# Kernel tuning notes

Measured on AMD Instinct MI355X. Metric: run time of the kernel, lower is better.

The kernel has to match this reference:

```python
import jax, jax.numpy as jnp
import numpy as np
from math import sqrt

B, S, H, NH = 4, 1024, 1024, 16
HS = H // NH
ALPHA = 2.0


def apply_rope(x, dis):
    # x: [B,S,NH,HS], dis: [B,S,1,HS] = [sin || cos]
    dis_sin, dis_cos = jnp.split(dis, 2, axis=-1)
    x0, x1 = x[..., 0::2], x[..., 1::2]
    return jnp.concatenate([x0 * dis_cos - x1 * dis_sin,
                            x1 * dis_cos + x0 * dis_sin], axis=-1)


def setup_inputs() -> dict:
    key = jax.random.key(0)
    ks = jax.random.split(key, 12)
    tgt = jax.random.normal(ks[0], (B, S, H), dtype=jnp.float32)
    # causal mask so every softmax row has at least one valid key
    tgt_mask = jnp.tril(jnp.ones((S, S), dtype=bool))[None, None]  # [1,1,S,S]
    tgt_mask = jnp.broadcast_to(tgt_mask, (B, 1, S, S))
    glycan_mass = jax.random.uniform(ks[1], (B, S, 1, HS), dtype=jnp.float32)
    glycan_query_mass = jax.random.uniform(ks[2], (B, S, 1, HS), dtype=jnp.float32)
    s = 1.0 / np.sqrt(H)
    Wq = jax.random.normal(ks[3], (H, H), dtype=jnp.float32) * s
    Wk = jax.random.normal(ks[4], (H, H), dtype=jnp.float32) * s
    Wv = jax.random.normal(ks[5], (H, H), dtype=jnp.float32) * (0.5 * s)  # beta gain
    Wo = jax.random.normal(ks[6], (H, H), dtype=jnp.float32) * (0.5 * s)
    bq = jnp.zeros((H,), jnp.float32)
    bk = jnp.zeros((H,), jnp.float32)
    bv = jnp.zeros((H,), jnp.float32)
    bo = jnp.zeros((H,), jnp.float32)
    ln_w = jnp.ones((H,), jnp.float32)
    ln_b = jnp.zeros((H,), jnp.float32)
    return {"tgt": tgt, "tgt_mask": tgt_mask, "glycan_mass": glycan_mass,
            "glycan_query_mass": glycan_query_mass,
            "Wq": Wq, "bq": bq, "Wk": Wk, "bk": bk, "Wv": Wv, "bv": bv,
            "Wo": Wo, "bo": bo, "ln_w": ln_w, "ln_b": ln_b}


def reference(tgt, tgt_mask, glycan_mass, glycan_query_mass,
              Wq, bq, Wk, bk, Wv, bv, Wo, bo, ln_w, ln_b):
    b = tgt.shape[0]
    q = (tgt @ Wq + bq).reshape(b, -1, NH, HS)
    k = (tgt @ Wk + bk).reshape(b, -1, NH, HS)
    v = (tgt @ Wv + bv).reshape(b, -1, NH, HS)
    q = apply_rope(q, glycan_query_mass)
    k = apply_rope(k, glycan_mass)
    # attn: [b, head, q_pos, k_pos]
    attn = jnp.einsum('bnij,bmij->binm', q, k) / sqrt(HS)
    attn = jnp.where(tgt_mask, attn, -jnp.inf)
    attn = jax.nn.softmax(attn, axis=-1)
    postx = jnp.einsum('binm,bmij->bnij', attn, v).reshape(b, -1, H)
    postx = postx @ Wo + bo
    # DeepNorm (dropout = identity at inference)
    x = tgt * ALPHA + postx
    mu = jnp.mean(x, axis=-1, keepdims=True)
    var = jnp.var(x, axis=-1, keepdims=True)
    return (x - mu) / jnp.sqrt(var + 1e-5) * ln_w + ln_b
```

## Files before the change

kernel.cpp:

```cpp
#include <hip/hip_runtime.h>

#define NB 4
#define NS 1024
#define NHID 1024
#define NHEAD 16
#define HDIM 64

typedef unsigned short u16;
typedef __bf16 bf16x8 __attribute__((ext_vector_type(8)));
typedef float f32x4 __attribute__((ext_vector_type(4)));
typedef u16 us8 __attribute__((ext_vector_type(8)));
typedef u16 us4 __attribute__((ext_vector_type(4)));

__device__ __forceinline__ u16 f2b(float f) {
  union { float f; unsigned u; } v; v.f = f;
  unsigned r = v.u + 0x7fffu + ((v.u >> 16) & 1u);
  return (u16)(r >> 16);
}
__device__ __forceinline__ float b2f(u16 b) {
  union { unsigned u; float f; } v; v.u = ((unsigned)b) << 16;
  return v.f;
}
__device__ __forceinline__ bf16x8 as_bf(us8 v) {
  bf16x8 r; __builtin_memcpy(&r, &v, sizeof(r)); return r;
}

__global__ void k_wt(const float* __restrict__ Wq, const float* __restrict__ Wk,
                     const float* __restrict__ Wv, const float* __restrict__ Wo,
                     u16* __restrict__ out) {
  const float* W = (blockIdx.z == 0) ? Wq : (blockIdx.z == 1) ? Wk
                   : (blockIdx.z == 2) ? Wv : Wo;
  u16* o = out + (size_t)blockIdx.z * NHID * NHID;
  __shared__ u16 tl[64][65];
  const int n0 = blockIdx.x * 64, k0 = blockIdx.y * 64;
  const int tr = threadIdx.x >> 4, tc = (threadIdx.x & 15) * 4;
#pragma unroll
  for (int rr = tr; rr < 64; rr += 16) {
    float4 v = *(const float4*)(W + (size_t)(k0 + rr) * NHID + n0 + tc);
    tl[rr][tc + 0] = f2b(v.x);
    tl[rr][tc + 1] = f2b(v.y);
    tl[rr][tc + 2] = f2b(v.z);
    tl[rr][tc + 3] = f2b(v.w);
  }
  __syncthreads();
#pragma unroll
  for (int rr = tr; rr < 64; rr += 16) {
    us4 v;
    v[0] = tl[tc + 0][rr];
    v[1] = tl[tc + 1][rr];
    v[2] = tl[tc + 2][rr];
    v[3] = tl[tc + 3][rr];
    *(us4*)(o + (size_t)(n0 + rr) * NHID + k0 + tc) = v;
  }
}

__global__ __launch_bounds__(256, 2) void k_gemm_qkv(
    const float* __restrict__ tgt, const u16* __restrict__ Wt,
    const float* __restrict__ bq, const float* __restrict__ bk,
    const float* __restrict__ bv, u16* __restrict__ Qb, u16* __restrict__ Kb,
    u16* __restrict__ VTb) {
  const int z = blockIdx.z;
  const u16* Wz = Wt + (size_t)z * NHID * NHID;
  const float* bias = (z == 0) ? bq : (z == 1) ? bk : bv;
  const bool vt = (z == 2);
  const int m0 = (vt ? blockIdx.x : blockIdx.y) * 128;
  const int n0 = (vt ? blockIdx.y : blockIdx.x) * 128;

  __shared__ u16 As[128 * 64];
  __shared__ u16 Bs[128 * 64];

  const int t = threadIdx.x;
  const int w = t >> 6, lane = t & 63, lq = lane & 15, lk = lane >> 4;
  const int wm = (w >> 1) * 64, wn = (w & 1) * 64;

  f32x4 acc[4][4];
#pragma unroll
  for (int i = 0; i < 4; i++)
#pragma unroll
    for (int j = 0; j < 4; j++) acc[i][j] = (f32x4){0.f, 0.f, 0.f, 0.f};

  for (int k0 = 0; k0 < NHID; k0 += 64) {
    __syncthreads();
#pragma unroll
    for (int i = 0; i < 4; i++) {
      int idx = t + i * 256;
      int r = idx >> 3, ch = idx & 7;
      us8 va, vb;
      if (!vt) {
        const float* ap = tgt + (size_t)(m0 + r) * NHID + k0 + ch * 8;
        float4 a0 = *(const float4*)ap;
        float4 a1 = *(const float4*)(ap + 4);
        va[0] = f2b(a0.x); va[1] = f2b(a0.y); va[2] = f2b(a0.z); va[3] = f2b(a0.w);
        va[4] = f2b(a1.x); va[5] = f2b(a1.y); va[6] = f2b(a1.z); va[7] = f2b(a1.w);
        vb = *(const us8*)(Wz + (size_t)(n0 + r) * NHID + k0 + ch * 8);
      } else {
        va = *(const us8*)(Wz + (size_t)(m0 + r) * NHID + k0 + ch * 8);
        const float* bp = tgt + (size_t)(n0 + r) * NHID + k0 + ch * 8;
        float4 b0 = *(const float4*)bp;
        float4 b1 = *(const float4*)(bp + 4);
        vb[0] = f2b(b0.x); vb[1] = f2b(b0.y); vb[2] = f2b(b0.z); vb[3] = f2b(b0.w);
        vb[4] = f2b(b1.x); vb[5] = f2b(b1.y); vb[6] = f2b(b1.z); vb[7] = f2b(b1.w);
      }
      *(us8*)(As + r * 64 + ((ch ^ (r & 7)) << 3)) = va;
      *(us8*)(Bs + r * 64 + ((ch ^ (r & 7)) << 3)) = vb;
    }
    __syncthreads();
#pragma unroll
    for (int kk = 0; kk < 2; kk++) {
      bf16x8 af[4], bfv[4];
#pragma unroll
      for (int m = 0; m < 4; m++) {
        int r = wm + m * 16 + lq;
        int ch = kk * 4 + lk;
        af[m] = as_bf(*(const us8*)(As + r * 64 + ((ch ^ (r & 7)) << 3)));
      }
#pragma unroll
      for (int n = 0; n < 4; n++) {
        int r = wn + n * 16 + lq;
        int ch = kk * 4 + lk;
        bfv[n] = as_bf(*(const us8*)(Bs + r * 64 + ((ch ^ (r & 7)) << 3)));
      }
#pragma unroll
      for (int m = 0; m < 4; m++)
#pragma unroll
        for (int n = 0; n < 4; n++)
          acc[m][n] = __builtin_amdgcn_mfma_f32_16x16x32_bf16(af[m], bfv[n],
                                                              acc[m][n], 0, 0, 0);
    }
  }
  if (!vt) {
#pragma unroll
    for (int m = 0; m < 4; m++)
#pragma unroll
      for (int n = 0; n < 4; n++) {
        int gn = n0 + wn + n * 16 + lq;
        int h = gn >> 6, d = gn & 63;
        float bval = bias[gn];
#pragma unroll
        for (int r = 0; r < 4; r++) {
          int gm = m0 + wm + m * 16 + 4 * lk + r;
          int b = gm >> 10, s = gm & 1023;
          float v = acc[m][n][r] + bval;
          ((z == 0) ? Qb : Kb)[(((size_t)(b * NHEAD + h) * NS + s) << 6) + d] =
              f2b(v);
        }
      }
  } else {
#pragma unroll
    for (int m = 0; m < 4; m++)
#pragma unroll
      for (int n = 0; n < 4; n++) {
        int gn = n0 + wn + n * 16 + lq;
        int b = gn >> 10, s = gn & 1023;
#pragma unroll
        for (int r = 0; r < 4; r++) {
          int gm = m0 + wm + m * 16 + 4 * lk + r;
          int h = gm >> 6, d = gm & 63;
          float v = acc[m][n][r] + bias[gm];
          VTb[(((size_t)(b * NHEAD + h)) << 16) + ((size_t)d << 10) + s] = f2b(v);
        }
      }
  }
}

__global__ void k_rope(u16* __restrict__ Qb, u16* __restrict__ Kb,
                       const float* __restrict__ qmass,
                       const float* __restrict__ kmass) {
  int id = blockIdx.x * 256 + threadIdx.x;
  int which = id >> 16;
  int r = id & 65535;
  int s = r & 1023;
  int b = r >> 14;
  u16* ptr = (which ? Kb : Qb) + ((size_t)r << 6);
  const float* dis = (which ? kmass : qmass) + ((size_t)(b * NS + s) << 6);
  float x[64];
#pragma unroll
  for (int c8 = 0; c8 < 8; c8++) {
    us8 v = *(const us8*)(ptr + c8 * 8);
#pragma unroll
    for (int j = 0; j < 8; j++) x[c8 * 8 + j] = b2f(v[j]);
  }
  us8 outv[8];
#pragma unroll
  for (int c = 0; c < 32; c++) {
    float sn = dis[c], cs = dis[32 + c];
    float x0 = x[2 * c], x1 = x[2 * c + 1];
    outv[c >> 3][c & 7] = f2b(x0 * cs - x1 * sn);
    outv[(c >> 3) + 4][c & 7] = f2b(x1 * cs + x0 * sn);
  }
#pragma unroll
  for (int c8 = 0; c8 < 8; c8++) *(us8*)(ptr + c8 * 8) = outv[c8];
}

__global__ __launch_bounds__(256, 2) void k_attn(const u16* __restrict__ Qb,
                                                 const u16* __restrict__ Kb,
                                                 const u16* __restrict__ VTb,
                                                 u16* __restrict__ Ob) {
  const int id = blockIdx.x;
  const int wrk = (id & 7) * 128 + (id >> 3);
  const int bh = wrk >> 4;
  const int qt = 15 - (wrk & 15);
  const int b = bh >> 4, h = bh & 15;
  const size_t hoff = (size_t)bh << 16;
  const u16* Qh = Qb + hoff;
  const u16* Kh = Kb + hoff;
  const u16* VTh = VTb + hoff;

  __shared__ u16 Ps[4][1024];

  const int t = threadIdx.x, w = t >> 6, lane = t & 63;
  const int lq = lane & 15, lk = lane >> 4;

  bf16x8 qf[2];
  {
    const u16* qr = Qh + (size_t)(qt * 64 + w * 16 + lq) * 64;
    qf[0] = as_bf(*(const us8*)(qr + lk * 8));
    qf[1] = as_bf(*(const us8*)(qr + 32 + lk * 8));
  }

  f32x4 oacc[4];
#pragma unroll
  for (int i = 0; i < 4; i++) oacc[i] = (f32x4){0.f, 0.f, 0.f, 0.f};
  float mrun[4] = {-1e30f, -1e30f, -1e30f, -1e30f};
  float lrun[4] = {0.f, 0.f, 0.f, 0.f};

  for (int kt = 0; kt <= qt; ++kt) {
    const u16* kb = Kh + ((size_t)kt << 12);
    us8 kfr[4][2];
#pragma unroll
    for (int fc = 0; fc < 4; fc++)
#pragma unroll
      for (int kk = 0; kk < 2; kk++)
        kfr[fc][kk] =
            *(const us8*)(kb + (fc * 16 + lq) * 64 + (kk * 4 + lk) * 8);
    us8 vfr[4][2];
#pragma unroll
    for (int fc = 0; fc < 4; fc++)
#pragma unroll
      for (int kk = 0; kk < 2; kk++)
        vfr[fc][kk] = *(const us8*)(VTh + ((size_t)(fc * 16 + lq) << 10) +
                                    kt * 64 + (kk * 4 + lk) * 8);

    f32x4 sfr[4];
#pragma unroll
    for (int fc = 0; fc < 4; fc++) {
      f32x4 a = (f32x4){0.f, 0.f, 0.f, 0.f};
#pragma unroll
      for (int kk = 0; kk < 2; kk++)
        a = __builtin_amdgcn_mfma_f32_16x16x32_bf16(qf[kk], as_bf(kfr[fc][kk]),
                                                    a, 0, 0, 0);
      sfr[fc] = a;
    }
    const float sc = 0.125f;
    if (kt == qt) {
#pragma unroll
      for (int fc = 0; fc < 4; fc++)
#pragma unroll
        for (int r = 0; r < 4; r++) {
          int qrow = w * 16 + 4 * lk + r;
          int kcol = fc * 16 + lq;
          sfr[fc][r] = (kcol <= qrow) ? sfr[fc][r] * sc : -1e30f;
        }
    } else {
#pragma unroll
      for (int fc = 0; fc < 4; fc++)
#pragma unroll
        for (int r = 0; r < 4; r++) sfr[fc][r] *= sc;
    }
    float pv[4][4];
#pragma unroll
    for (int r = 0; r < 4; r++) {
      float mx = fmaxf(fmaxf(sfr[0][r], sfr[1][r]), fmaxf(sfr[2][r], sfr[3][r]));
#pragma unroll
      for (int d = 1; d < 16; d <<= 1) mx = fmaxf(mx, __shfl_xor(mx, d));
      float mn = fmaxf(mrun[r], mx);
      float corr = __expf(mrun[r] - mn);
      float rs = 0.f;
#pragma unroll
      for (int fc = 0; fc < 4; fc++) {
        float p = __expf(sfr[fc][r] - mn);
        pv[fc][r] = p;
        rs += p;
      }
#pragma unroll
      for (int d = 1; d < 16; d <<= 1) rs += __shfl_xor(rs, d);
      mrun[r] = mn;
      lrun[r] = lrun[r] * corr + rs;
#pragma unroll
      for (int fc = 0; fc < 4; fc++) oacc[fc][r] *= corr;
    }
    u16* Pw = Ps[w];
#pragma unroll
    for (int fc = 0; fc < 4; fc++)
#pragma unroll
      for (int r = 0; r < 4; r++) {
        int i = 4 * lk + r, c = fc * 16 + lq;
        Pw[i * 64 + (((c >> 3) ^ (i & 7)) << 3) + (c & 7)] = f2b(pv[fc][r]);
      }
    bf16x8 pf[2];
#pragma unroll
    for (int kk = 0; kk < 2; kk++) {
      int ch = kk * 4 + lk;
      pf[kk] = as_bf(*(const us8*)(Pw + lq * 64 + ((ch ^ (lq & 7)) << 3)));
    }
#pragma unroll
    for (int fc = 0; fc < 4; fc++)
#pragma unroll
      for (int kk = 0; kk < 2; kk++)
        oacc[fc] = __builtin_amdgcn_mfma_f32_16x16x32_bf16(
            pf[kk], as_bf(vfr[fc][kk]), oacc[fc], 0, 0, 0);
  }
#pragma unroll
  for (int fc = 0; fc < 4; fc++)
#pragma unroll
    for (int r = 0; r < 4; r++) {
      int qrow = qt * 64 + w * 16 + 4 * lk + r;
      float o = oacc[fc][r] / lrun[r];
      Ob[((size_t)(b * NS + qrow) << 10) + h * 64 + fc * 16 + lq] = f2b(o);
    }
}

__global__ __launch_bounds__(256, 2) void k_gemm_o(
    const u16* __restrict__ Ab, const u16* __restrict__ Wz,
    const float* __restrict__ bo, const float* __restrict__ tgt,
    u16* __restrict__ xb) {
  __shared__ u16 As[128 * 64];
  __shared__ u16 Bs[128 * 64];

  const int t = threadIdx.x;
  const int m0 = blockIdx.y * 128, n0 = blockIdx.x * 128;
  const int w = t >> 6, lane = t & 63, lq = lane & 15, lk = lane >> 4;
  const int wm = (w >> 1) * 64, wn = (w & 1) * 64;

  f32x4 acc[4][4];
#pragma unroll
  for (int i = 0; i < 4; i++)
#pragma unroll
    for (int j = 0; j < 4; j++) acc[i][j] = (f32x4){0.f, 0.f, 0.f, 0.f};

  for (int k0 = 0; k0 < NHID; k0 += 64) {
    __syncthreads();
#pragma unroll
    for (int i = 0; i < 4; i++) {
      int idx = t + i * 256;
      int r = idx >> 3, ch = idx & 7;
      us8 va = *(const us8*)(Ab + (size_t)(m0 + r) * NHID + k0 + ch * 8);
      *(us8*)(As + r * 64 + ((ch ^ (r & 7)) << 3)) = va;
      us8 vb = *(const us8*)(Wz + (size_t)(n0 + r) * NHID + k0 + ch * 8);
      *(us8*)(Bs + r * 64 + ((ch ^ (r & 7)) << 3)) = vb;
    }
    __syncthreads();
#pragma unroll
    for (int kk = 0; kk < 2; kk++) {
      bf16x8 af[4], bfv[4];
#pragma unroll
      for (int m = 0; m < 4; m++) {
        int r = wm + m * 16 + lq;
        int ch = kk * 4 + lk;
        af[m] = as_bf(*(const us8*)(As + r * 64 + ((ch ^ (r & 7)) << 3)));
      }
#pragma unroll
      for (int n = 0; n < 4; n++) {
        int r = wn + n * 16 + lq;
        int ch = kk * 4 + lk;
        bfv[n] = as_bf(*(const us8*)(Bs + r * 64 + ((ch ^ (r & 7)) << 3)));
      }
#pragma unroll
      for (int m = 0; m < 4; m++)
#pragma unroll
        for (int n = 0; n < 4; n++)
          acc[m][n] = __builtin_amdgcn_mfma_f32_16x16x32_bf16(af[m], bfv[n],
                                                              acc[m][n], 0, 0, 0);
    }
  }
#pragma unroll
  for (int m = 0; m < 4; m++)
#pragma unroll
    for (int n = 0; n < 4; n++) {
      int gn = n0 + wn + n * 16 + lq;
      float bval = bo[gn];
#pragma unroll
      for (int r = 0; r < 4; r++) {
        int gm = m0 + wm + m * 16 + 4 * lk + r;
        float v = acc[m][n][r] + bval + 2.0f * tgt[((size_t)gm << 10) + gn];
        xb[((size_t)gm << 10) + gn] = f2b(v);
      }
    }
}

__global__ void k_ln(const u16* __restrict__ xb, const float* __restrict__ lw,
                     const float* __restrict__ lb, float* __restrict__ out) {
  const int row = blockIdx.x, t = threadIdx.x;
  const u16* xr = xb + ((size_t)row << 10);
  us4 v = *(const us4*)(xr + t * 4);
  float f[4];
  float s = 0.f, sq = 0.f;
#pragma unroll
  for (int j = 0; j < 4; j++) {
    f[j] = b2f(v[j]);
    s += f[j];
    sq += f[j] * f[j];
  }
#pragma unroll
  for (int d = 1; d < 64; d <<= 1) {
    s += __shfl_xor(s, d);
    sq += __shfl_xor(sq, d);
  }
  __shared__ float ss[4], sk[4];
  int w = t >> 6, lane = t & 63;
  if (lane == 0) {
    ss[w] = s;
    sk[w] = sq;
  }
  __syncthreads();
  s = ss[0] + ss[1] + ss[2] + ss[3];
  sq = sk[0] + sk[1] + sk[2] + sk[3];
  float mean = s * (1.0f / 1024.0f);
  float var = sq * (1.0f / 1024.0f) - mean * mean;
  float rstd = rsqrtf(var + 1e-5f);
  float4 o;
#pragma unroll
  for (int j = 0; j < 4; j++) {
    int c = t * 4 + j;
    ((float*)&o)[j] = (f[j] - mean) * rstd * lw[c] + lb[c];
  }
  *(float4*)(out + ((size_t)row << 10) + t * 4) = o;
}

extern "C" void kernel_launch(void* const* d_in, const int* in_sizes, int n_in,
                              void* d_out, int out_size, void* d_ws,
                              size_t ws_size, hipStream_t stream) {
  const float* tgt = (const float*)d_in[0];
  const float* kmass = (const float*)d_in[2];
  const float* qmass = (const float*)d_in[3];
  const float* Wq = (const float*)d_in[4];
  const float* bq = (const float*)d_in[5];
  const float* Wk = (const float*)d_in[6];
  const float* bk = (const float*)d_in[7];
  const float* Wv = (const float*)d_in[8];
  const float* bv = (const float*)d_in[9];
  const float* Wo = (const float*)d_in[10];
  const float* bo = (const float*)d_in[11];
  const float* lw = (const float*)d_in[12];
  const float* lb = (const float*)d_in[13];
  float* out = (float*)d_out;

  char* ws = (char*)d_ws;
  u16* Wt = (u16*)ws;
  u16* Qb = (u16*)(ws + (8u << 20));
  u16* Kb = (u16*)(ws + (16u << 20));
  u16* VTb = (u16*)(ws + (24u << 20));
  u16* Ob = (u16*)(ws + (32u << 20));
  u16* xb = (u16*)(ws + (8u << 20));

  k_wt<<<dim3(16, 16, 4), 256, 0, stream>>>(Wq, Wk, Wv, Wo, Wt);
  k_gemm_qkv<<<dim3(8, 32, 3), 256, 0, stream>>>(tgt, Wt, bq, bk, bv, Qb, Kb,
                                                 VTb);
  k_rope<<<512, 256, 0, stream>>>(Qb, Kb, qmass, kmass);
  k_attn<<<1024, 256, 0, stream>>>(Qb, Kb, VTb, Ob);
  k_gemm_o<<<dim3(8, 32), 256, 0, stream>>>(Ob, Wt + 3u * NHID * NHID, bo, tgt,
                                            xb);
  k_ln<<<4096, 256, 0, stream>>>(xb, lw, lb, out);
}
```

Measured before the change: 304.5 us.

## Transpose attention MFMA operands so each lane owns one query row

The attention kernel swaps the MFMA operand order so the score and output tiles are transposed, with each lane holding a single query row. Row max and sum reductions then need two cross-lane shuffles instead of four per row, the per-row softmax state shrinks to scalars, and P is written to shared memory as packed 8-byte stores. Work is also split per wave on 16-row query tiles rather than per block on 64-row tiles, so each wave stops at its own causal bound and finishes with vectorized output stores. In exchange, waves in one block run loops of different lengths, and K/V fragments are still reloaded from global memory by every wave.

```diff
diff --git a/kernel.cpp b/kernel.cpp
--- a/kernel.cpp
+++ b/kernel.cpp
@@ -198,22 +198,24 @@
                                                  u16* __restrict__ Ob) {
   const int id = blockIdx.x;
   const int wrk = (id & 7) * 128 + (id >> 3);
-  const int bh = wrk >> 4;
-  const int qt = 15 - (wrk & 15);
+  const int w = threadIdx.x >> 6, lane = threadIdx.x & 63;
+  const int item = wrk * 4 + w;
+  const int bh = item >> 6;
+  const int qt16 = 63 - (item & 63);
   const int b = bh >> 4, h = bh & 15;
   const size_t hoff = (size_t)bh << 16;
   const u16* Qh = Qb + hoff;
   const u16* Kh = Kb + hoff;
   const u16* VTh = VTb + hoff;
-
-  __shared__ u16 Ps[4][1024];
-
-  const int t = threadIdx.x, w = t >> 6, lane = t & 63;
   const int lq = lane & 15, lk = lane >> 4;
+
+  __shared__ u16 Ps[4 * 16 * 64];
+  char* Prow = (char*)(Ps + (w * 16 + lq) * 64);
+  const unsigned swz = (unsigned)((lq & 7) << 4);
 
   bf16x8 qf[2];
   {
-    const u16* qr = Qh + (size_t)(qt * 64 + w * 16 + lq) * 64;
+    const u16* qr = Qh + (size_t)(qt16 * 16 + lq) * 64;
     qf[0] = as_bf(*(const us8*)(qr + lk * 8));
     qf[1] = as_bf(*(const us8*)(qr + 32 + lk * 8));
   }
@@ -221,10 +223,13 @@
   f32x4 oacc[4];
 #pragma unroll
   for (int i = 0; i < 4; i++) oacc[i] = (f32x4){0.f, 0.f, 0.f, 0.f};
-  float mrun[4] = {-1e30f, -1e30f, -1e30f, -1e30f};
-  float lrun[4] = {0.f, 0.f, 0.f, 0.f};
-
-  for (int kt = 0; kt <= qt; ++kt) {
+  float mrun = -1e30f, lrun = 0.f;
+
+  const int ktmax = qt16 >> 2;
+  const int qg = qt16 * 16 + lq;
+  const float sc = 0.125f;
+
+  for (int kt = 0; kt <= ktmax; ++kt) {
     const u16* kb = Kh + ((size_t)kt << 12);
     us8 kfr[4][2];
 #pragma unroll
@@ -232,14 +237,14 @@
 #pragma unroll
       for (int kk = 0; kk < 2; kk++)
         kfr[fc][kk] =
-            *(const us8*)(kb + (fc * 16 + lq) * 64 + (kk * 4 + lk) * 8);
+            *(const us8*)(kb + (fc * 16 + lq) * 64 + kk * 32 + lk * 8);
     us8 vfr[4][2];
 #pragma unroll
     for (int fc = 0; fc < 4; fc++)
 #pragma unroll
       for (int kk = 0; kk < 2; kk++)
         vfr[fc][kk] = *(const us8*)(VTh + ((size_t)(fc * 16 + lq) << 10) +
-                                    kt * 64 + (kk * 4 + lk) * 8);
+                                    kt * 64 + kk * 32 + lk * 8);
 
     f32x4 sfr[4];
 #pragma unroll
@@ -247,19 +252,17 @@
       f32x4 a = (f32x4){0.f, 0.f, 0.f, 0.f};
 #pragma unroll
       for (int kk = 0; kk < 2; kk++)
-        a = __builtin_amdgcn_mfma_f32_16x16x32_bf16(qf[kk], as_bf(kfr[fc][kk]),
+        a = __builtin_amdgcn_mfma_f32_16x16x32_bf16(as_bf(kfr[fc][kk]), qf[kk],
                                                     a, 0, 0, 0);
       sfr[fc] = a;
     }
-    const float sc = 0.125f;
-    if (kt == qt) {
+    if (kt == ktmax) {
 #pragma unroll
       for (int fc = 0; fc < 4; fc++)
 #pragma unroll
         for (int r = 0; r < 4; r++) {
-          int qrow = w * 16 + 4 * lk + r;
-          int kcol = fc * 16 + lq;
-          sfr[fc][r] = (kcol <= qrow) ? sfr[fc][r] * sc : -1e30f;
+          int kg = kt * 64 + fc * 16 + 4 * lk + r;
+          sfr[fc][r] = (kg <= qg) ? sfr[fc][r] * sc : -1e30f;
         }
     } else {
 #pragma unroll
@@ -267,57 +270,61 @@
 #pragma unroll
         for (int r = 0; r < 4; r++) sfr[fc][r] *= sc;
     }
-    float pv[4][4];
-#pragma unroll
-    for (int r = 0; r < 4; r++) {
-      float mx = fmaxf(fmaxf(sfr[0][r], sfr[1][r]), fmaxf(sfr[2][r], sfr[3][r]));
-#pragma unroll
-      for (int d = 1; d < 16; d <<= 1) mx = fmaxf(mx, __shfl_xor(mx, d));
-      float mn = fmaxf(mrun[r], mx);
-      float corr = __expf(mrun[r] - mn);
-      float rs = 0.f;
-#pragma unroll
-      for (int fc = 0; fc < 4; fc++) {
+    float tm = sfr[0][0];
+#pragma unroll
+    for (int fc = 0; fc < 4; fc++)
+#pragma unroll
+      for (int r = 0; r < 4; r++) tm = fmaxf(tm, sfr[fc][r]);
+    tm = fmaxf(tm, __shfl_xor(tm, 16));
+    tm = fmaxf(tm, __shfl_xor(tm, 32));
+    const float mn = fmaxf(mrun, tm);
+    const float corr = __expf(mrun - mn);
+    mrun = mn;
+    float pvv[4][4];
+    float rs = 0.f;
+#pragma unroll
+    for (int fc = 0; fc < 4; fc++)
+#pragma unroll
+      for (int r = 0; r < 4; r++) {
         float p = __expf(sfr[fc][r] - mn);
-        pv[fc][r] = p;
+        pvv[fc][r] = p;
         rs += p;
       }
-#pragma unroll
-      for (int d = 1; d < 16; d <<= 1) rs += __shfl_xor(rs, d);
-      mrun[r] = mn;
-      lrun[r] = lrun[r] * corr + rs;
-#pragma unroll
-      for (int fc = 0; fc < 4; fc++) oacc[fc][r] *= corr;
-    }
-    u16* Pw = Ps[w];
-#pragma unroll
-    for (int fc = 0; fc < 4; fc++)
-#pragma unroll
-      for (int r = 0; r < 4; r++) {
-        int i = 4 * lk + r, c = fc * 16 + lq;
-        Pw[i * 64 + (((c >> 3) ^ (i & 7)) << 3) + (c & 7)] = f2b(pv[fc][r]);
-      }
+    rs += __shfl_xor(rs, 16);
+    rs += __shfl_xor(rs, 32);
+    lrun = lrun * corr + rs;
+#pragma unroll
+    for (int fc = 0; fc < 4; fc++) oacc[fc] *= corr;
+
+#pragma unroll
+    for (int fc = 0; fc < 4; fc++) {
+      uint2 pk;
+      pk.x = (unsigned)f2b(pvv[fc][0]) | ((unsigned)f2b(pvv[fc][1]) << 16);
+      pk.y = (unsigned)f2b(pvv[fc][2]) | ((unsigned)f2b(pvv[fc][3]) << 16);
+      *(uint2*)(Prow + (((unsigned)(fc * 32 + lk * 8)) ^ swz)) = pk;
+    }
     bf16x8 pf[2];
 #pragma unroll
-    for (int kk = 0; kk < 2; kk++) {
-      int ch = kk * 4 + lk;
-      pf[kk] = as_bf(*(const us8*)(Pw + lq * 64 + ((ch ^ (lq & 7)) << 3)));
-    }
+    for (int kk = 0; kk < 2; kk++)
+      pf[kk] = as_bf(
+          *(const us8*)(Prow + (((unsigned)(kk * 64 + lk * 16)) ^ swz)));
+
 #pragma unroll
     for (int fc = 0; fc < 4; fc++)
 #pragma unroll
       for (int kk = 0; kk < 2; kk++)
         oacc[fc] = __builtin_amdgcn_mfma_f32_16x16x32_bf16(
-            pf[kk], as_bf(vfr[fc][kk]), oacc[fc], 0, 0, 0);
-  }
-#pragma unroll
-  for (int fc = 0; fc < 4; fc++)
-#pragma unroll
-    for (int r = 0; r < 4; r++) {
-      int qrow = qt * 64 + w * 16 + 4 * lk + r;
-      float o = oacc[fc][r] / lrun[r];
-      Ob[((size_t)(b * NS + qrow) << 10) + h * 64 + fc * 16 + lq] = f2b(o);
-    }
+            as_bf(vfr[fc][kk]), pf[kk], oacc[fc], 0, 0, 0);
+  }
+  const float inv = 1.0f / lrun;
+  u16* orow = Ob + ((size_t)(b * NS + qg) << 10) + h * 64;
+#pragma unroll
+  for (int fc = 0; fc < 4; fc++) {
+    us4 st;
+#pragma unroll
+    for (int r = 0; r < 4; r++) st[r] = f2b(oacc[fc][r] * inv);
+    *(us4*)(orow + fc * 16 + 4 * lk) = st;
+  }
 }
 
 __global__ __launch_bounds__(256, 2) void k_gemm_o(
```

New measurement: 322.7 us. +6.0%, slower.
